# Optimization experiments

Measured on AMD Instinct MI355X. Metric: run time of the kernel, lower is better.

The kernel has to match this reference:

```python
import jax, jax.numpy as jnp
import numpy as np

# Finite-difference stencils along a given axis with one-sided boundary handling:
#  'f' : forward diff  d[i]=(X[i+1]-X[i])/h, last voxel copies previous diff
#  'b' : backward diff d[i]=(X[i]-X[i-1])/h, first voxel copies next diff
#  'c' : central diff  d[i]=(X[i+1]-X[i-1])/(2h), one-sided at boundaries

def _g(X, axis, h, kind):
    Xm = jnp.moveaxis(X, axis, 0)
    d = (Xm[1:] - Xm[:-1]) / h  # length n-1 one-step diffs
    if kind == 'f':
        r = jnp.concatenate([d, d[-1:]], axis=0)
    elif kind == 'b':
        r = jnp.concatenate([d[:1], d], axis=0)
    else:  # central
        r = jnp.concatenate([d[:1], (Xm[2:] - Xm[:-2]) / (2.0 * h), d[-1:]], axis=0)
    return jnp.moveaxis(r, 0, axis)

HX = HY = HZ = 1.0  # data_spacing = [1,1,1]

dXc = lambda X: _g(X, 1, HX, 'c')
dYc = lambda X: _g(X, 2, HY, 'c')
dZc = lambda X: _g(X, 3, HZ, 'c')
dXf = lambda X: _g(X, 1, HX, 'f')
dYf = lambda X: _g(X, 2, HY, 'f')
dZf = lambda X: _g(X, 3, HZ, 'f')
dXb = lambda X: _g(X, 1, HX, 'b')
dYb = lambda X: _g(X, 2, HY, 'b')
dZb = lambda X: _g(X, 3, HZ, 'b')


def setup_inputs() -> dict:
    key = jax.random.key(0)
    ks = jax.random.split(key, 10)
    shp = (2, 160, 160, 160)
    f32 = jnp.float32
    return {
        'C':   jax.random.normal(ks[0], shp, f32),
        'Vx':  jax.random.normal(ks[1], shp, f32),
        'Vy':  jax.random.normal(ks[2], shp, f32),
        'Vz':  jax.random.normal(ks[3], shp, f32),
        'Dxx': jax.random.uniform(ks[4], shp, f32),
        'Dxy': jax.random.normal(ks[5], shp, f32) * 0.1,
        'Dxz': jax.random.normal(ks[6], shp, f32) * 0.1,
        'Dyy': jax.random.uniform(ks[7], shp, f32),
        'Dyz': jax.random.normal(ks[8], shp, f32) * 0.1,
        'Dzz': jax.random.uniform(ks[9], shp, f32),
    }


def reference(C, Vx, Vy, Vz, Dxx, Dxy, Dxz, Dyy, Dyz, Dzz):
    # --- diffusion term: Grad_fullD (3D, full symmetric tensor D) ---
    Cx_c, Cy_c, Cz_c = dXc(C), dYc(C), dZc(C)        # central grads of C
    Cx_f, Cy_f, Cz_f = dXf(C), dYf(C), dZf(C)        # forward grads of C
    diff = ((dXc(Dxx) + dYc(Dxy) + dZc(Dxz)) * Cx_c
            + (dXc(Dxy) + dYc(Dyy) + dZc(Dyz)) * Cy_c
            + (dXc(Dxz) + dYc(Dyz) + dZc(Dzz)) * Cz_c
            + Dxx * dXb(Cx_f) + Dyy * dYb(Cy_f) + Dzz * dZb(Cz_f)
            + Dxy * (dXb(Cy_f) + dYb(Cx_f))
            + Dyz * (dYb(Cz_f) + dZb(Cy_f))
            + Dxz * (dZb(Cx_f) + dXb(Cz_f)))
    # --- advection term: Grad_vectorV (upwind per-voxel on sign of V) ---
    C_x = jnp.where(Vx > 0, dXb(C), dXf(C))
    C_y = jnp.where(Vy > 0, dYb(C), dYf(C))
    C_z = jnp.where(Vz > 0, dZb(C), dZf(C))
    adv = -(Vx * C_x + Vy * C_y + Vz * C_z) - C * (dXc(Vx) + dYc(Vy) + dZc(Vz))
    return diff + adv
```

## Files before the change

### kernel.cpp

```cpp
#include <hip/hip_runtime.h>

#define N   160
#define SZl 1
#define SYl 160
#define SXl (160*160)

__global__ __launch_bounds__(640) void piano_energy_kernel(
    const float* __restrict__ C,   const float* __restrict__ Vx,
    const float* __restrict__ Vy,  const float* __restrict__ Vz,
    const float* __restrict__ Dxx, const float* __restrict__ Dxy,
    const float* __restrict__ Dxz, const float* __restrict__ Dyy,
    const float* __restrict__ Dyz, const float* __restrict__ Dzz,
    float* __restrict__ out)
{
    const int z = threadIdx.x;
    const int y = blockIdx.y * 4 + threadIdx.y;
    const int x = blockIdx.x;
    const int b = blockIdx.z;

    const int idx = ((b * N + x) * N + y) * N + z;

    const int oxp = (x < N - 1) ?  SXl : 0;
    const int oxm = (x > 0)     ? -SXl : 0;
    const int oyp = (y < N - 1) ?  SYl : 0;
    const int oym = (y > 0)     ? -SYl : 0;
    const int ozp = (z < N - 1) ?  SZl : 0;
    const int ozm = (z > 0)     ? -SZl : 0;

    const float sx = (x == 0 || x == N - 1) ? 1.f : 0.5f;
    const float sy = (y == 0 || y == N - 1) ? 1.f : 0.5f;
    const float sz = (z == 0 || z == N - 1) ? 1.f : 0.5f;

    const float c0  = C[idx];
    const float cxp = C[idx + oxp], cxm = C[idx + oxm];
    const float cyp = C[idx + oyp], cym = C[idx + oym];
    const float czp = C[idx + ozp], czm = C[idx + ozm];

    const float Cx_c = sx * (cxp - cxm);
    const float Cy_c = sy * (cyp - cym);
    const float Cz_c = sz * (czp - czm);
    const float Cx_f = (x < N - 1) ? (cxp - c0) : (c0 - cxm);
    const float Cy_f = (y < N - 1) ? (cyp - c0) : (c0 - cym);
    const float Cz_f = (z < N - 1) ? (czp - c0) : (c0 - czm);
    const float Cx_b = (x > 0) ? (c0 - cxm) : (cxp - c0);
    const float Cy_b = (y > 0) ? (c0 - cym) : (cyp - c0);
    const float Cz_b = (z > 0) ? (c0 - czm) : (czp - c0);

    float sXX, sYY, sZZ;
    if (x == 0)          sXX = C[idx + 2 * SXl] - 2.f * cxp + c0;
    else if (x == N - 1) sXX = 0.f;
    else                 sXX = cxp - 2.f * c0 + cxm;
    if (y == 0)          sYY = C[idx + 2 * SYl] - 2.f * cyp + c0;
    else if (y == N - 1) sYY = 0.f;
    else                 sYY = cyp - 2.f * c0 + cym;
    if (z == 0)          sZZ = C[idx + 2 * SZl] - 2.f * czp + c0;
    else if (z == N - 1) sZZ = 0.f;
    else                 sZZ = czp - 2.f * c0 + czm;

    const int ofxp = oxp;                       const int ofx0 = (x == N - 1) ? -SXl : 0;
    const int ofyp = oyp;                       const int ofy0 = (y == N - 1) ? -SYl : 0;
    const int ofzp = ozp;                       const int ofz0 = (z == N - 1) ? -SZl : 0;
    const int obx1 = (x > 0) ? 0 : SXl;         const int obx0 = obx1 - SXl;
    const int oby1 = (y > 0) ? 0 : SYl;         const int oby0 = oby1 - SYl;
    const int obz1 = (z > 0) ? 0 : SZl;         const int obz0 = obz1 - SZl;

    const float crossXY = (C[idx + obx1 + ofyp] - C[idx + obx1 + ofy0])
                        - (C[idx + obx0 + ofyp] - C[idx + obx0 + ofy0]);
    const float crossYX = (C[idx + oby1 + ofxp] - C[idx + oby1 + ofx0])
                        - (C[idx + oby0 + ofxp] - C[idx + oby0 + ofx0]);
    const float crossYZ = (C[idx + oby1 + ofzp] - C[idx + oby1 + ofz0])
                        - (C[idx + oby0 + ofzp] - C[idx + oby0 + ofz0]);
    const float crossZY = (C[idx + obz1 + ofyp] - C[idx + obz1 + ofy0])
                        - (C[idx + obz0 + ofyp] - C[idx + obz0 + ofy0]);
    const float crossZX = (C[idx + obz1 + ofxp] - C[idx + obz1 + ofx0])
                        - (C[idx + obz0 + ofxp] - C[idx + obz0 + ofx0]);
    const float crossXZ = (C[idx + obx1 + ofzp] - C[idx + obx1 + ofz0])
                        - (C[idx + obx0 + ofzp] - C[idx + obx0 + ofz0]);

    const float dDxx_x = sx * (Dxx[idx + oxp] - Dxx[idx + oxm]);
    const float dDxy_x = sx * (Dxy[idx + oxp] - Dxy[idx + oxm]);
    const float dDxy_y = sy * (Dxy[idx + oyp] - Dxy[idx + oym]);
    const float dDxz_x = sx * (Dxz[idx + oxp] - Dxz[idx + oxm]);
    const float dDxz_z = sz * (Dxz[idx + ozp] - Dxz[idx + ozm]);
    const float dDyy_y = sy * (Dyy[idx + oyp] - Dyy[idx + oym]);
    const float dDyz_y = sy * (Dyz[idx + oyp] - Dyz[idx + oym]);
    const float dDyz_z = sz * (Dyz[idx + ozp] - Dyz[idx + ozm]);
    const float dDzz_z = sz * (Dzz[idx + ozp] - Dzz[idx + ozm]);

    const float t1 = dDxx_x + dDxy_y + dDxz_z;
    const float t2 = dDxy_x + dDyy_y + dDyz_z;
    const float t3 = dDxz_x + dDyz_y + dDzz_z;

    const float Dxx0 = Dxx[idx], Dyy0 = Dyy[idx], Dzz0 = Dzz[idx];
    const float Dxy0 = Dxy[idx], Dyz0 = Dyz[idx], Dxz0 = Dxz[idx];

    const float diff = t1 * Cx_c + t2 * Cy_c + t3 * Cz_c
                     + Dxx0 * sXX + Dyy0 * sYY + Dzz0 * sZZ
                     + Dxy0 * (crossXY + crossYX)
                     + Dyz0 * (crossYZ + crossZY)
                     + Dxz0 * (crossZX + crossXZ);

    const float Vx0 = Vx[idx], Vy0 = Vy[idx], Vz0 = Vz[idx];
    const float dVx = sx * (Vx[idx + oxp] - Vx[idx + oxm]);
    const float dVy = sy * (Vy[idx + oyp] - Vy[idx + oym]);
    const float dVz = sz * (Vz[idx + ozp] - Vz[idx + ozm]);

    const float C_x = (Vx0 > 0.f) ? Cx_b : Cx_f;
    const float C_y = (Vy0 > 0.f) ? Cy_b : Cy_f;
    const float C_z = (Vz0 > 0.f) ? Cz_b : Cz_f;

    const float adv = -(Vx0 * C_x + Vy0 * C_y + Vz0 * C_z)
                    - c0 * (dVx + dVy + dVz);

    out[idx] = diff + adv;
}

extern "C" void kernel_launch(void* const* d_in, const int* in_sizes, int n_in,
                              void* d_out, int out_size, void* d_ws, size_t ws_size,
                              hipStream_t stream) {
    const float* C   = (const float*)d_in[0];
    const float* Vx  = (const float*)d_in[1];
    const float* Vy  = (const float*)d_in[2];
    const float* Vz  = (const float*)d_in[3];
    const float* Dxx = (const float*)d_in[4];
    const float* Dxy = (const float*)d_in[5];
    const float* Dxz = (const float*)d_in[6];
    const float* Dyy = (const float*)d_in[7];
    const float* Dyz = (const float*)d_in[8];
    const float* Dzz = (const float*)d_in[9];
    float* out = (float*)d_out;

    dim3 grid(N, N / 4, 2);
    dim3 block(N, 4, 1);
    hipLaunchKernelGGL(piano_energy_kernel, grid, block, 0, stream,
                       C, Vx, Vy, Vz, Dxx, Dxy, Dxz, Dyy, Dyz, Dzz, out);
}
```

Before: 358.3 us.

## Process four z-voxels per thread with float4 loads and register z-stencil reuse

Each thread now computes four consecutive z voxels, using float4 vector loads for all arrays and reusing loaded values in registers for the z-direction neighbours and cross-derivative terms. The block shape becomes 40x8 to match. This cuts the number of load instructions and the redundant scalar gathers of the original one-voxel-per-thread stencil. The cost is higher register pressure and more complex boundary logic for the z edges. It also adds unaligned halo scalar loads at the ends of each four-voxel chunk.

Result: slower. 387.0 us (+8.0%).

```diff
diff --git a/kernel.cpp b/kernel.cpp
--- a/kernel.cpp
+++ b/kernel.cpp
@@ -1,11 +1,27 @@
 #include <hip/hip_runtime.h>
 
-#define N   160
-#define SZl 1
-#define SYl 160
-#define SXl (160*160)
-
-__global__ __launch_bounds__(640) void piano_energy_kernel(
+#define N  160
+#define SX (N * N)
+#define SY N
+
+typedef float f4 __attribute__((ext_vector_type(4)));
+
+__device__ __forceinline__ f4 ld4(const float* __restrict__ p) {
+    return *(const f4* __restrict__)p;
+}
+
+struct A6 { float v[6]; };
+
+__device__ __forceinline__ A6 ld6(const float* __restrict__ p, int base, int tx) {
+    A6 a;
+    f4 c = ld4(p + base);
+    a.v[1] = c.x; a.v[2] = c.y; a.v[3] = c.z; a.v[4] = c.w;
+    a.v[0] = (tx > 0)  ? p[base - 1] : c.x;
+    a.v[5] = (tx < 39) ? p[base + 4] : c.w;
+    return a;
+}
+
+__global__ __launch_bounds__(320) void piano_energy_kernel(
     const float* __restrict__ C,   const float* __restrict__ Vx,
     const float* __restrict__ Vy,  const float* __restrict__ Vz,
     const float* __restrict__ Dxx, const float* __restrict__ Dxy,
@@ -13,106 +29,184 @@
     const float* __restrict__ Dyz, const float* __restrict__ Dzz,
     float* __restrict__ out)
 {
-    const int z = threadIdx.x;
-    const int y = blockIdx.y * 4 + threadIdx.y;
-    const int x = blockIdx.x;
-    const int b = blockIdx.z;
-
-    const int idx = ((b * N + x) * N + y) * N + z;
-
-    const int oxp = (x < N - 1) ?  SXl : 0;
-    const int oxm = (x > 0)     ? -SXl : 0;
-    const int oyp = (y < N - 1) ?  SYl : 0;
-    const int oym = (y > 0)     ? -SYl : 0;
-    const int ozp = (z < N - 1) ?  SZl : 0;
-    const int ozm = (z > 0)     ? -SZl : 0;
-
-    const float sx = (x == 0 || x == N - 1) ? 1.f : 0.5f;
-    const float sy = (y == 0 || y == N - 1) ? 1.f : 0.5f;
-    const float sz = (z == 0 || z == N - 1) ? 1.f : 0.5f;
-
-    const float c0  = C[idx];
-    const float cxp = C[idx + oxp], cxm = C[idx + oxm];
-    const float cyp = C[idx + oyp], cym = C[idx + oym];
-    const float czp = C[idx + ozp], czm = C[idx + ozm];
-
-    const float Cx_c = sx * (cxp - cxm);
-    const float Cy_c = sy * (cyp - cym);
-    const float Cz_c = sz * (czp - czm);
-    const float Cx_f = (x < N - 1) ? (cxp - c0) : (c0 - cxm);
-    const float Cy_f = (y < N - 1) ? (cyp - c0) : (c0 - cym);
-    const float Cz_f = (z < N - 1) ? (czp - c0) : (c0 - czm);
-    const float Cx_b = (x > 0) ? (c0 - cxm) : (cxp - c0);
-    const float Cy_b = (y > 0) ? (c0 - cym) : (cyp - c0);
-    const float Cz_b = (z > 0) ? (c0 - czm) : (czp - c0);
-
-    float sXX, sYY, sZZ;
-    if (x == 0)          sXX = C[idx + 2 * SXl] - 2.f * cxp + c0;
-    else if (x == N - 1) sXX = 0.f;
-    else                 sXX = cxp - 2.f * c0 + cxm;
-    if (y == 0)          sYY = C[idx + 2 * SYl] - 2.f * cyp + c0;
-    else if (y == N - 1) sYY = 0.f;
-    else                 sYY = cyp - 2.f * c0 + cym;
-    if (z == 0)          sZZ = C[idx + 2 * SZl] - 2.f * czp + c0;
-    else if (z == N - 1) sZZ = 0.f;
-    else                 sZZ = czp - 2.f * c0 + czm;
-
-    const int ofxp = oxp;                       const int ofx0 = (x == N - 1) ? -SXl : 0;
-    const int ofyp = oyp;                       const int ofy0 = (y == N - 1) ? -SYl : 0;
-    const int ofzp = ozp;                       const int ofz0 = (z == N - 1) ? -SZl : 0;
-    const int obx1 = (x > 0) ? 0 : SXl;         const int obx0 = obx1 - SXl;
-    const int oby1 = (y > 0) ? 0 : SYl;         const int oby0 = oby1 - SYl;
-    const int obz1 = (z > 0) ? 0 : SZl;         const int obz0 = obz1 - SZl;
-
-    const float crossXY = (C[idx + obx1 + ofyp] - C[idx + obx1 + ofy0])
-                        - (C[idx + obx0 + ofyp] - C[idx + obx0 + ofy0]);
-    const float crossYX = (C[idx + oby1 + ofxp] - C[idx + oby1 + ofx0])
-                        - (C[idx + oby0 + ofxp] - C[idx + oby0 + ofx0]);
-    const float crossYZ = (C[idx + oby1 + ofzp] - C[idx + oby1 + ofz0])
-                        - (C[idx + oby0 + ofzp] - C[idx + oby0 + ofz0]);
-    const float crossZY = (C[idx + obz1 + ofyp] - C[idx + obz1 + ofy0])
-                        - (C[idx + obz0 + ofyp] - C[idx + obz0 + ofy0]);
-    const float crossZX = (C[idx + obz1 + ofxp] - C[idx + obz1 + ofx0])
-                        - (C[idx + obz0 + ofxp] - C[idx + obz0 + ofx0]);
-    const float crossXZ = (C[idx + obx1 + ofzp] - C[idx + obx1 + ofz0])
-                        - (C[idx + obx0 + ofzp] - C[idx + obx0 + ofz0]);
-
-    const float dDxx_x = sx * (Dxx[idx + oxp] - Dxx[idx + oxm]);
-    const float dDxy_x = sx * (Dxy[idx + oxp] - Dxy[idx + oxm]);
-    const float dDxy_y = sy * (Dxy[idx + oyp] - Dxy[idx + oym]);
-    const float dDxz_x = sx * (Dxz[idx + oxp] - Dxz[idx + oxm]);
-    const float dDxz_z = sz * (Dxz[idx + ozp] - Dxz[idx + ozm]);
-    const float dDyy_y = sy * (Dyy[idx + oyp] - Dyy[idx + oym]);
-    const float dDyz_y = sy * (Dyz[idx + oyp] - Dyz[idx + oym]);
-    const float dDyz_z = sz * (Dyz[idx + ozp] - Dyz[idx + ozm]);
-    const float dDzz_z = sz * (Dzz[idx + ozp] - Dzz[idx + ozm]);
-
-    const float t1 = dDxx_x + dDxy_y + dDxz_z;
-    const float t2 = dDxy_x + dDyy_y + dDyz_z;
-    const float t3 = dDxz_x + dDyz_y + dDzz_z;
-
-    const float Dxx0 = Dxx[idx], Dyy0 = Dyy[idx], Dzz0 = Dzz[idx];
-    const float Dxy0 = Dxy[idx], Dyz0 = Dyz[idx], Dxz0 = Dxz[idx];
-
-    const float diff = t1 * Cx_c + t2 * Cy_c + t3 * Cz_c
-                     + Dxx0 * sXX + Dyy0 * sYY + Dzz0 * sZZ
-                     + Dxy0 * (crossXY + crossYX)
-                     + Dyz0 * (crossYZ + crossZY)
-                     + Dxz0 * (crossZX + crossXZ);
-
-    const float Vx0 = Vx[idx], Vy0 = Vy[idx], Vz0 = Vz[idx];
-    const float dVx = sx * (Vx[idx + oxp] - Vx[idx + oxm]);
-    const float dVy = sy * (Vy[idx + oyp] - Vy[idx + oym]);
-    const float dVz = sz * (Vz[idx + ozp] - Vz[idx + ozm]);
-
-    const float C_x = (Vx0 > 0.f) ? Cx_b : Cx_f;
-    const float C_y = (Vy0 > 0.f) ? Cy_b : Cy_f;
-    const float C_z = (Vz0 > 0.f) ? Cz_b : Cz_f;
-
-    const float adv = -(Vx0 * C_x + Vy0 * C_y + Vz0 * C_z)
-                    - c0 * (dVx + dVy + dVz);
-
-    out[idx] = diff + adv;
+    const int tx = threadIdx.x;
+    const int zb = tx * 4;
+    const int y  = blockIdx.y * 8 + threadIdx.y;
+    const int x  = blockIdx.x;
+    const int b  = blockIdx.z;
+    const int idx = ((b * N + x) * N + y) * N + zb;
+
+    const bool xlo = (x > 0), xhi = (x < N - 1);
+    const bool ylo = (y > 0), yhi = (y < N - 1);
+
+    const int oxp = xhi ? SX : 0,  oxm = xlo ? -SX : 0;
+    const int oyp = yhi ? SY : 0,  oym = ylo ? -SY : 0;
+    const float sxs = (xlo && xhi) ? 0.5f : 1.f;
+    const float sys = (ylo && yhi) ? 0.5f : 1.f;
+
+    const int obx1 = xlo ? 0 : SX,  obx0 = obx1 - SX;
+    const int oby1 = ylo ? 0 : SY,  oby0 = oby1 - SY;
+    const int ofxp = oxp,           ofx0 = xhi ? 0 : -SX;
+    const int ofyp = oyp,           ofy0 = yhi ? 0 : -SY;
+
+    f4 xyA = ld4(C + idx + obx1 + ofyp);
+    f4 xyB = ld4(C + idx + obx1 + ofy0);
+    f4 xyC = ld4(C + idx + obx0 + ofyp);
+    f4 xyD = ld4(C + idx + obx0 + ofy0);
+    f4 yxA = ld4(C + idx + oby1 + ofxp);
+    f4 yxB = ld4(C + idx + oby1 + ofx0);
+    f4 yxC = ld4(C + idx + oby0 + ofxp);
+    f4 yxD = ld4(C + idx + oby0 + ofx0);
+
+    float cXY[4];
+#pragma unroll
+    for (int j = 0; j < 4; ++j)
+        cXY[j] = (xyA[j] - xyB[j]) - (xyC[j] - xyD[j])
+               + (yxA[j] - yxB[j]) - (yxC[j] - yxD[j]);
+
+    A6 cc  = ld6(C, idx,       tx);
+    A6 cxp = ld6(C, idx + oxp, tx);
+    A6 cxm = ld6(C, idx + oxm, tx);
+    A6 cyp = ld6(C, idx + oyp, tx);
+    A6 cym = ld6(C, idx + oym, tx);
+
+    f4 cx2 = 0, cy2 = 0;
+    if (x == 0) cx2 = ld4(C + idx + 2 * SX);
+    if (y == 0) cy2 = ld4(C + idx + 2 * SY);
+
+    float gX[6], gY[6];
+#pragma unroll
+    for (int k = 0; k < 6; ++k) {
+        gX[k] = xhi ? (cxp.v[k] - cc.v[k]) : (cc.v[k] - cxm.v[k]);
+        gY[k] = yhi ? (cyp.v[k] - cc.v[k]) : (cc.v[k] - cym.v[k]);
+    }
+
+    float c0[4], fxp[4], fxm[4], fyp[4], fym[4], fzp[4], fzm[4];
+    float Cxc[4], Cyc[4], Czc[4], sXX[4], sYY[4], sZZ[4], cXZ[4], cYZ[4];
+
+#pragma unroll
+    for (int j = 0; j < 4; ++j) {
+        const int z = zb + j;
+        const bool zbot = (z == 0), ztop = (z == N - 1);
+
+        c0[j]  = cc.v[j + 1];
+        fxp[j] = cxp.v[j + 1]; fxm[j] = cxm.v[j + 1];
+        fyp[j] = cyp.v[j + 1]; fym[j] = cym.v[j + 1];
+        fzp[j] = cc.v[j + 2];  fzm[j] = cc.v[j];
+
+        const float szs = (zbot || ztop) ? 1.f : 0.5f;
+        Cxc[j] = sxs * (fxp[j] - fxm[j]);
+        Cyc[j] = sys * (fyp[j] - fym[j]);
+        Czc[j] = szs * (fzp[j] - fzm[j]);
+
+        sXX[j] = !xhi ? 0.f : (xlo ? (fxp[j] - 2.f * c0[j] + fxm[j])
+                                   : (cx2[j] - 2.f * fxp[j] + c0[j]));
+        sYY[j] = !yhi ? 0.f : (ylo ? (fyp[j] - 2.f * c0[j] + fym[j])
+                                   : (cy2[j] - 2.f * fyp[j] + c0[j]));
+        sZZ[j] = ztop ? 0.f : (!zbot ? (fzp[j] - 2.f * c0[j] + fzm[j])
+                                     : (cc.v[3] - 2.f * cc.v[2] + cc.v[1]));
+
+        const float zx = zbot ? (gX[j + 2] - gX[j + 1]) : (gX[j + 1] - gX[j]);
+        const float zy = zbot ? (gY[j + 2] - gY[j + 1]) : (gY[j + 1] - gY[j]);
+
+#define FZD(P) (ztop ? (P.v[j + 1] - P.v[j]) : (P.v[j + 2] - P.v[j + 1]))
+        const float xz = xlo ? (FZD(cc) - FZD(cxm)) : (FZD(cxp) - FZD(cc));
+        const float yz = ylo ? (FZD(cc) - FZD(cym)) : (FZD(cyp) - FZD(cc));
+#undef FZD
+        cXZ[j] = zx + xz;
+        cYZ[j] = zy + yz;
+    }
+
+    float res[4];
+    {
+        f4 vxc = ld4(Vx + idx), vxp = ld4(Vx + idx + oxp), vxm = ld4(Vx + idx + oxm);
+        f4 vyc = ld4(Vy + idx), vyp = ld4(Vy + idx + oyp), vym = ld4(Vy + idx + oym);
+        A6 vz6 = ld6(Vz, idx, tx);
+#pragma unroll
+        for (int j = 0; j < 4; ++j) {
+            const int z = zb + j;
+            const bool zbot = (z == 0), ztop = (z == N - 1);
+            const float szs = (zbot || ztop) ? 1.f : 0.5f;
+
+            const float dVx = sxs * (vxp[j] - vxm[j]);
+            const float dVy = sys * (vyp[j] - vym[j]);
+            const float dVz = szs * (vz6.v[j + 2] - vz6.v[j]);
+
+            const float Cxf = xhi  ? (fxp[j] - c0[j]) : (c0[j] - fxm[j]);
+            const float Cxb = xlo  ? (c0[j] - fxm[j]) : (fxp[j] - c0[j]);
+            const float Cyf = yhi  ? (fyp[j] - c0[j]) : (c0[j] - fym[j]);
+            const float Cyb = ylo  ? (c0[j] - fym[j]) : (fyp[j] - c0[j]);
+            const float Czf = ztop ? (c0[j] - fzm[j]) : (fzp[j] - c0[j]);
+            const float Czb = zbot ? (fzp[j] - c0[j]) : (c0[j] - fzm[j]);
+
+            const float C_x = (vxc[j] > 0.f) ? Cxb : Cxf;
+            const float C_y = (vyc[j] > 0.f) ? Cyb : Cyf;
+            const float C_z = (vz6.v[j + 1] > 0.f) ? Czb : Czf;
+
+            res[j] = -(vxc[j] * C_x + vyc[j] * C_y + vz6.v[j + 1] * C_z)
+                   - c0[j] * (dVx + dVy + dVz);
+        }
+    }
+
+    {
+        f4 dc = ld4(Dxx + idx), dp = ld4(Dxx + idx + oxp), dm = ld4(Dxx + idx + oxm);
+#pragma unroll
+        for (int j = 0; j < 4; ++j)
+            res[j] += sxs * (dp[j] - dm[j]) * Cxc[j] + dc[j] * sXX[j];
+    }
+    {
+        f4 dc = ld4(Dyy + idx), dp = ld4(Dyy + idx + oyp), dm = ld4(Dyy + idx + oym);
+#pragma unroll
+        for (int j = 0; j < 4; ++j)
+            res[j] += sys * (dp[j] - dm[j]) * Cyc[j] + dc[j] * sYY[j];
+    }
+    {
+        A6 d6 = ld6(Dzz, idx, tx);
+#pragma unroll
+        for (int j = 0; j < 4; ++j) {
+            const int z = zb + j;
+            const float szs = (z == 0 || z == N - 1) ? 1.f : 0.5f;
+            res[j] += szs * (d6.v[j + 2] - d6.v[j]) * Czc[j] + d6.v[j + 1] * sZZ[j];
+        }
+    }
+    {
+        f4 dc = ld4(Dxy + idx);
+        f4 dxp = ld4(Dxy + idx + oxp), dxm = ld4(Dxy + idx + oxm);
+        f4 dyp = ld4(Dxy + idx + oyp), dym = ld4(Dxy + idx + oym);
+#pragma unroll
+        for (int j = 0; j < 4; ++j)
+            res[j] += sxs * (dxp[j] - dxm[j]) * Cyc[j]
+                    + sys * (dyp[j] - dym[j]) * Cxc[j]
+                    + dc[j] * cXY[j];
+    }
+    {
+        A6 d6 = ld6(Dxz, idx, tx);
+        f4 dp = ld4(Dxz + idx + oxp), dm = ld4(Dxz + idx + oxm);
+#pragma unroll
+        for (int j = 0; j < 4; ++j) {
+            const int z = zb + j;
+            const float szs = (z == 0 || z == N - 1) ? 1.f : 0.5f;
+            res[j] += sxs * (dp[j] - dm[j]) * Czc[j]
+                    + szs * (d6.v[j + 2] - d6.v[j]) * Cxc[j]
+                    + d6.v[j + 1] * cXZ[j];
+        }
+    }
+    {
+        A6 d6 = ld6(Dyz, idx, tx);
+        f4 dp = ld4(Dyz + idx + oyp), dm = ld4(Dyz + idx + oym);
+#pragma unroll
+        for (int j = 0; j < 4; ++j) {
+            const int z = zb + j;
+            const float szs = (z == 0 || z == N - 1) ? 1.f : 0.5f;
+            res[j] += sys * (dp[j] - dm[j]) * Czc[j]
+                    + szs * (d6.v[j + 2] - d6.v[j]) * Cyc[j]
+                    + d6.v[j + 1] * cYZ[j];
+        }
+    }
+
+    f4 o;
+    o.x = res[0]; o.y = res[1]; o.z = res[2]; o.w = res[3];
+    *(f4*)(out + idx) = o;
 }
 
 extern "C" void kernel_launch(void* const* d_in, const int* in_sizes, int n_in,
@@ -130,8 +224,8 @@
     const float* Dzz = (const float*)d_in[9];
     float* out = (float*)d_out;
 
-    dim3 grid(N, N / 4, 2);
-    dim3 block(N, 4, 1);
+    dim3 grid(N, N / 8, 2);
+    dim3 block(N / 4, 8, 1);
     hipLaunchKernelGGL(piano_energy_kernel, grid, block, 0, stream,
                        C, Vx, Vy, Vz, Dxx, Dxy, Dxz, Dyy, Dyz, Dzz, out);
 }
```
